# Optimization experiments

Hardware: AMD Instinct MI355X
Metric: run time of the kernel (lower is better)

The kernel has to match this reference:

```python
import jax, jax.numpy as jnp
import numpy as np

B, T, C = 4, 2048, 1024
H = 16
D = C // H  # head_dim = 64


def setup_inputs() -> dict:
    key = jax.random.key(0)
    k1, k2, k3, k4, k5 = jax.random.split(key, 5)
    s = 1.0 / np.sqrt(C)
    return {
        "hidden_state": jax.random.normal(k1, (B, T, C), dtype=jnp.float32),
        "qkv_w": jax.random.uniform(k2, (C, 3 * C), jnp.float32, -s, s),
        "qkv_b": jax.random.uniform(k3, (3 * C,), jnp.float32, -s, s),
        "o_w": jax.random.uniform(k4, (C, C), jnp.float32, -s, s),
        "o_b": jax.random.uniform(k5, (C,), jnp.float32, -s, s),
    }


def reference(hidden_state, qkv_w, qkv_b, o_w, o_b):
    Bq, Tq, Cq = hidden_state.shape
    qkv = hidden_state @ qkv_w + qkv_b  # [B,T,3C]
    q, k, v = jnp.split(qkv, 3, axis=-1)
    # [B,T,C] -> [B,H,T,D]
    q = q.reshape(Bq, Tq, H, D).transpose(0, 2, 1, 3)
    k = k.reshape(Bq, Tq, H, D).transpose(0, 2, 1, 3)
    v = v.reshape(Bq, Tq, H, D).transpose(0, 2, 1, 3)
    scaling = D ** (-0.5)
    scores = jnp.einsum("bhqd,bhkd->bhqk", q, k) * scaling  # [B,H,T,T]
    causal = jnp.tril(jnp.ones((Tq, Tq), dtype=bool))
    scores = jnp.where(causal[None, None], scores, -jnp.inf)
    attn = jax.nn.softmax(scores, axis=-1)
    out = jnp.einsum("bhqk,bhkd->bhqd", attn, v)  # [B,H,T,D]
    out = out.transpose(0, 2, 1, 3).reshape(Bq, Tq, Cq)
    return out @ o_w + o_b
```

## Files before the change

### kernel.cpp

```cpp
#include <hip/hip_runtime.h>
#include <hip/hip_bf16.h>

#define Bn 4
#define Tn 2048
#define Cn 1024
#define Hn 16
#define Dn 64
#define Kdim 1024

typedef __bf16 bf16x8 __attribute__((ext_vector_type(8)));
typedef float f32x4 __attribute__((ext_vector_type(4)));
union B8 { uint4 u; bf16x8 f; ushort s[8]; };

static __device__ __forceinline__ ushort f2bf(float x) {
    __hip_bfloat16 h = __float2bfloat16(x);
    return *(ushort*)&h;
}

#define AS1 __attribute__((address_space(1)))
#define AS3 __attribute__((address_space(3)))

static __device__ __forceinline__ void gload_lds16(const ushort* g, ushort* l) {
    __builtin_amdgcn_global_load_lds((AS1 const uint4*)(const void*)g,
                                     (AS3 uint4*)(void*)l, 16, 0, 0);
}

__global__ __launch_bounds__(256) void prep_fused(
    const float* __restrict__ X, const float* __restrict__ qkv_w,
    const float* __restrict__ o_w,
    ushort* __restrict__ Xb, ushort* __restrict__ Wqt, ushort* __restrict__ Wot)
{
    if (blockIdx.y == 0) {
        int i = (blockIdx.x * 256 + threadIdx.x) * 8;
        float4 a = *(const float4*)&X[i];
        float4 b = *(const float4*)&X[i + 4];
        ushort4 o0, o1;
        o0.x = f2bf(a.x); o0.y = f2bf(a.y); o0.z = f2bf(a.z); o0.w = f2bf(a.w);
        o1.x = f2bf(b.x); o1.y = f2bf(b.y); o1.z = f2bf(b.z); o1.w = f2bf(b.w);
        *(ushort4*)&Xb[i] = o0;
        *(ushort4*)&Xb[i + 4] = o1;
        return;
    }
    const float* W; ushort* Wt; int N, bx;
    if (blockIdx.y == 1) { W = qkv_w; Wt = Wqt; N = 3 * Cn; bx = blockIdx.x; }
    else                 { W = o_w;   Wt = Wot; N = Cn;     bx = blockIdx.x; }
    if (bx >= (N / 32) * 32) return;
    const int n0 = (bx % (N / 32)) * 32, k0 = (bx / (N / 32)) * 32;
    __shared__ float Ls[32][33];
    const int tx = threadIdx.x & 31, ty = threadIdx.x >> 5;
    #pragma unroll
    for (int i = 0; i < 4; i++) {
        int r = ty + i * 8;
        Ls[r][tx] = W[(size_t)(k0 + r) * N + n0 + tx];
    }
    __syncthreads();
    #pragma unroll
    for (int i = 0; i < 4; i++) {
        int r = ty + i * 8;
        Wt[(size_t)(n0 + r) * Kdim + k0 + tx] = f2bf(Ls[tx][r]);
    }
}

template <int EPI>
__global__ __launch_bounds__(256) void gemm_bt(
    const ushort* __restrict__ A, const ushort* __restrict__ Bt,
    const float* __restrict__ bias,
    float* __restrict__ Out, ushort* __restrict__ Qb,
    ushort* __restrict__ Kb, ushort* __restrict__ Vtb)
{
    const int m0 = blockIdx.y * 128;
    const int n0 = blockIdx.x * 128;
    const int t  = threadIdx.x;
    const int wave = t >> 6, lane = t & 63;
    const int ln = lane & 15, quad = lane >> 4;
    const int wm = wave >> 1, wn = wave & 1;

    __shared__ ushort As[128 * 64];
    __shared__ ushort Bs[128 * 64];

    f32x4 acc[4][4] = {};

    for (int k0 = 0; k0 < Kdim; k0 += 64) {
        __syncthreads();
        #pragma unroll
        for (int it = 0; it < 4; it++) {
            int c = it * 256 + wave * 64 + lane;
            int row = c >> 3, seg = c & 7;
            int gseg = seg ^ (row & 7);
            gload_lds16(&A [(size_t)(m0 + row) * Kdim + k0 + gseg * 8], &As[c * 8]);
            gload_lds16(&Bt[(size_t)(n0 + row) * Kdim + k0 + gseg * 8], &Bs[c * 8]);
        }
        __syncthreads();

        #pragma unroll
        for (int ks = 0; ks < 2; ks++) {
            bf16x8 af[4], bf[4];
            #pragma unroll
            for (int mm = 0; mm < 4; mm++) {
                int row = wm * 64 + mm * 16 + ln;
                int seg = (ks * 4 + quad) ^ (ln & 7);
                B8 tmp; tmp.u = *(const uint4*)&As[row * 64 + seg * 8];
                af[mm] = tmp.f;
            }
            #pragma unroll
            for (int nn = 0; nn < 4; nn++) {
                int row = wn * 64 + nn * 16 + ln;
                int seg = (ks * 4 + quad) ^ (ln & 7);
                B8 tmp; tmp.u = *(const uint4*)&Bs[row * 64 + seg * 8];
                bf[nn] = tmp.f;
            }
            #pragma unroll
            for (int mm = 0; mm < 4; mm++)
                #pragma unroll
                for (int nn = 0; nn < 4; nn++)
                    acc[mm][nn] = __builtin_amdgcn_mfma_f32_16x16x32_bf16(
                        af[mm], bf[nn], acc[mm][nn], 0, 0, 0);
        }
    }

    if (EPI == 0) {
        #pragma unroll
        for (int nn = 0; nn < 4; nn++) {
            int n = n0 + wn * 64 + nn * 16 + ln;
            float bv = bias[n];
            #pragma unroll
            for (int mm = 0; mm < 4; mm++) {
                int mbase = m0 + wm * 64 + mm * 16 + quad * 4;
                #pragma unroll
                for (int reg = 0; reg < 4; reg++)
                    Out[(size_t)(mbase + reg) * 1024 + n] = acc[mm][nn][reg] + bv;
            }
        }
    } else {
        const int nb = n0 + wn * 64;
        const int which = nb >> 10;
        const int h = (nb & 1023) >> 6;
        const float scale = (which == 0) ? 0.125f * 1.44269504088896f : 1.0f;
        const int b_ = m0 >> 11;
        const int t0 = (m0 & 2047) + wm * 64;

        __syncthreads();
        ushort* tile = ((wave & 2) ? Bs : As) + (wave & 1) * 4096;

        if (which == 2) {
            #pragma unroll
            for (int nn = 0; nn < 4; nn++) {
                float bv = bias[nb + nn * 16 + ln];
                #pragma unroll
                for (int mm = 0; mm < 4; mm++)
                    #pragma unroll
                    for (int reg = 0; reg < 4; reg++) {
                        int m = mm * 16 + quad * 4 + reg;
                        int n = nn * 16 + ln;
                        tile[n * 64 + (m ^ (((n >> 1) & 7) * 8))] =
                            f2bf(acc[mm][nn][reg] + bv);
                    }
            }
            #pragma unroll
            for (int it = 0; it < 8; it++) {
                int idx = it * 64 + lane;
                int row = idx >> 3, seg = idx & 7;
                uint4 v = *(const uint4*)&tile[row * 64 +
                              ((seg * 8) ^ (((row >> 1) & 7) * 8))];
                *(uint4*)&Vtb[((size_t)((b_ * Hn + h) * Dn) + row) * Tn + t0 + seg * 8] = v;
            }
        } else {
            ushort* dst = (which == 0) ? Qb : Kb;
            #pragma unroll
            for (int nn = 0; nn < 4; nn++) {
                float bv = bias[nb + nn * 16 + ln];
                #pragma unroll
                for (int mm = 0; mm < 4; mm++)
                    #pragma unroll
                    for (int reg = 0; reg < 4; reg++) {
                        int m = mm * 16 + quad * 4 + reg;
                        int n = nn * 16 + ln;
                        tile[m * 64 + (n ^ (((m >> 1) & 7) * 8))] =
                            f2bf((acc[mm][nn][reg] + bv) * scale);
                    }
            }
            #pragma unroll
            for (int it = 0; it < 8; it++) {
                int idx = it * 64 + lane;
                int row = idx >> 3, seg = idx & 7;
                uint4 v = *(const uint4*)&tile[row * 64 +
                              ((seg * 8) ^ (((row >> 1) & 7) * 8))];
                *(uint4*)&dst[((size_t)((b_ * Hn + h) * Tn) + t0 + row) * Dn + seg * 8] = v;
            }
        }
    }
}

__global__ __launch_bounds__(256, 2) void attn_mfma(
    const ushort* __restrict__ Qb, const ushort* __restrict__ Kb,
    const ushort* __restrict__ Vtb, ushort* __restrict__ Ob)
{
    const int bh   = blockIdx.x;
    const int qt   = 15 - blockIdx.y;
    const int t    = threadIdx.x;
    const int wave = t >> 6, lane = t & 63;
    const int ln   = lane & 15, quad = lane >> 4;

    __shared__ ushort Ks[2][128 * 64];
    __shared__ ushort Ps[4][32 * 34];

    const ushort* KgB = Kb  + (size_t)bh * Tn * Dn;
    const ushort* VgB = Vtb + (size_t)bh * Dn * Tn;
    const int b_ = bh >> 4, h = bh & 15;

    #define STAGE_K(kc, buf)                                                   \
        do {                                                                   \
            _Pragma("unroll")                                                  \
            for (int it = 0; it < 4; it++) {                                   \
                int c = it * 256 + wave * 64 + lane;                           \
                int row = c >> 3, seg = c & 7;                                 \
                int gs = seg ^ (row & 7);                                      \
                gload_lds16(&KgB[(size_t)((kc) * 128 + row) * Dn + gs * 8],    \
                            &Ks[buf][c * 8]);                                  \
            }                                                                  \
        } while (0)

    int cur = 0;
    STAGE_K(0, 0);

    const int q0 = qt * 128;

    const ushort* Qg = Qb + ((size_t)bh * Tn + q0 + wave * 32) * Dn;
    bf16x8 qf[2][2];
    #pragma unroll
    for (int ns = 0; ns < 2; ns++)
        #pragma unroll
        for (int ks = 0; ks < 2; ks++) {
            B8 tmp; tmp.u = *(const uint4*)&Qg[(ns * 16 + ln) * 64 + ks * 32 + quad * 8];
            qf[ns][ks] = tmp.f;
        }

    f32x4 Oacc[4][2] = {};
    float m_r[2] = {-1e30f, -1e30f}, l_r[2] = {0.f, 0.f};

    for (int kc = 0; kc <= qt; kc++) {
        __syncthreads();

        B8 vfr[4][4];
        #pragma unroll
        for (int gks = 0; gks < 4; gks++)
            #pragma unroll
            for (int ctd = 0; ctd < 4; ctd++)
                vfr[ctd][gks].u = *(const uint4*)&VgB[
                    (size_t)(ctd * 16 + ln) * Tn + kc * 128 + gks * 32 + quad * 8];

        if (kc < qt) STAGE_K(kc + 1, cur ^ 1);

        const ushort* Kc = Ks[cur];
        f32x4 S[8][2] = {};
        #pragma unroll
        for (int ks = 0; ks < 2; ks++)
            #pragma unroll
            for (int ct = 0; ct < 8; ct++) {
                B8 a; a.u = *(const uint4*)&Kc[(ct * 16 + ln) * 64 +
                                               (((ks * 4 + quad) ^ (ln & 7)) * 8)];
                #pragma unroll
                for (int ns = 0; ns < 2; ns++)
                    S[ct][ns] = __builtin_amdgcn_mfma_f32_16x16x32_bf16(
                        a.f, qf[ns][ks], S[ct][ns], 0, 0, 0);
            }

        if (kc == qt) {
            #pragma unroll
            for (int ct = 0; ct < 8; ct++) {
                int keyl = ct * 16 + quad * 4;
                #pragma unroll
                for (int ns = 0; ns < 2; ns++) {
                    int ql = wave * 32 + ns * 16 + ln;
                    #pragma unroll
                    for (int reg = 0; reg < 4; reg++)
                        if (keyl + reg > ql) S[ct][ns][reg] = -1e30f;
                }
            }
        }

        float alpha[2], ssum[2] = {0.f, 0.f};
        #pragma unroll
        for (int ns = 0; ns < 2; ns++) {
            float pm = -1e30f;
            #pragma unroll
            for (int ct = 0; ct < 8; ct++)
                #pragma unroll
                for (int reg = 0; reg < 4; reg++)
                    pm = fmaxf(pm, S[ct][ns][reg]);
            pm = fmaxf(pm, __shfl_xor(pm, 16));
            pm = fmaxf(pm, __shfl_xor(pm, 32));
            float mn = fmaxf(m_r[ns], pm);
            alpha[ns] = exp2f(m_r[ns] - mn);
            m_r[ns] = mn;
            #pragma unroll
            for (int ctd = 0; ctd < 4; ctd++)
                Oacc[ctd][ns] *= alpha[ns];
        }

        ushort* Pw = Ps[wave];
        #pragma unroll
        for (int p = 0; p < 4; p++) {
            #pragma unroll
            for (int ct_h = 0; ct_h < 2; ct_h++) {
                int ct = p * 2 + ct_h;
                #pragma unroll
                for (int ns = 0; ns < 2; ns++) {
                    ushort4 o;
                    #pragma unroll
                    for (int reg = 0; reg < 4; reg++) {
                        float pv = exp2f(S[ct][ns][reg] - m_r[ns]);
                        ssum[ns] += pv;
                        ((ushort*)&o)[reg] = f2bf(pv);
                    }
                    *(ushort4*)&Pw[(ns * 16 + ln) * 34 + ct_h * 16 + quad * 4] = o;
                }
            }
            #pragma unroll
            for (int ns = 0; ns < 2; ns++) {
                B8 pfr; pfr.u = *(const uint4*)&Pw[(ns * 16 + ln) * 34 + quad * 8];
                #pragma unroll
                for (int ctd = 0; ctd < 4; ctd++)
                    Oacc[ctd][ns] = __builtin_amdgcn_mfma_f32_16x16x32_bf16(
                        vfr[ctd][p].f, pfr.f, Oacc[ctd][ns], 0, 0, 0);
            }
        }
        #pragma unroll
        for (int ns = 0; ns < 2; ns++) {
            float s = ssum[ns];
            s += __shfl_xor(s, 16);
            s += __shfl_xor(s, 32);
            l_r[ns] = l_r[ns] * alpha[ns] + s;
        }
        cur ^= 1;
    }

    #pragma unroll
    for (int ns = 0; ns < 2; ns++) {
        float inv = 1.0f / l_r[ns];
        int token = q0 + wave * 32 + ns * 16 + ln;
        ushort* dst = Ob + ((size_t)(b_ * Tn + token)) * Cn + h * 64;
        #pragma unroll
        for (int ctd = 0; ctd < 4; ctd++) {
            ushort4 o;
            #pragma unroll
            for (int reg = 0; reg < 4; reg++)
                ((ushort*)&o)[reg] = f2bf(Oacc[ctd][ns][reg] * inv);
            *(ushort4*)&dst[ctd * 16 + quad * 4] = o;
        }
    }
    #undef STAGE_K
}

extern "C" void kernel_launch(void* const* d_in, const int* in_sizes, int n_in,
                              void* d_out, int out_size, void* d_ws, size_t ws_size,
                              hipStream_t stream) {
    const float* X     = (const float*)d_in[0];
    const float* qkv_w = (const float*)d_in[1];
    const float* qkv_b = (const float*)d_in[2];
    const float* o_w   = (const float*)d_in[3];
    const float* o_b   = (const float*)d_in[4];
    float* out = (float*)d_out;

    const size_t BTC = (size_t)Bn * Tn * Cn;
    ushort* Xb  = (ushort*)d_ws;
    ushort* Wqt = Xb  + BTC;
    ushort* Wot = Wqt + 3 * Cn * Cn;
    ushort* Qb  = Wot + Cn * Cn;
    ushort* Kb  = Qb  + BTC;
    ushort* Vtb = Kb  + BTC;
    ushort* Ao  = Vtb + BTC;

    prep_fused<<<dim3(4096, 3), 256, 0, stream>>>(X, qkv_w, o_w, Xb, Wqt, Wot);

    gemm_bt<1><<<dim3(3 * Cn / 128, 8192 / 128), 256, 0, stream>>>(
        Xb, Wqt, qkv_b, nullptr, Qb, Kb, Vtb);
    attn_mfma<<<dim3(Bn * Hn, 16), 256, 0, stream>>>(Qb, Kb, Vtb, Ao);
    gemm_bt<0><<<dim3(Cn / 128, 8192 / 128), 256, 0, stream>>>(
        Ao, Wot, o_b, out, nullptr, nullptr, nullptr);
}
```

Before: 306.3 us.

## Pair causal query tiles per block, lazy rescale, MFMA row-sum

Each attention block now handles two query tiles, qt = 15-y and qt = y, so every block does the same amount of causal work, and the grid shrinks from 16 to 8 in y. The online-softmax rescale of the output accumulators is skipped unless the running max grows by more than a threshold, checked wave-wide. The softmax denominator is computed with an MFMA against a ones vector instead of scalar sums and shuffles. Risks: half as many blocks may reduce occupancy, and the lazy rescale allows exponentials larger than one in bf16.

Result: no change. 303.4 us (-0.9%).

```diff
diff --git a/kernel.cpp b/kernel.cpp
--- a/kernel.cpp
+++ b/kernel.cpp
@@ -196,7 +196,7 @@
     const ushort* __restrict__ Vtb, ushort* __restrict__ Ob)
 {
     const int bh   = blockIdx.x;
-    const int qt   = 15 - blockIdx.y;
+    const int yp   = blockIdx.y;
     const int t    = threadIdx.x;
     const int wave = t >> 6, lane = t & 63;
     const int ln   = lane & 15, quad = lane >> 4;
@@ -207,6 +207,10 @@
     const ushort* KgB = Kb  + (size_t)bh * Tn * Dn;
     const ushort* VgB = Vtb + (size_t)bh * Dn * Tn;
     const int b_ = bh >> 4, h = bh & 15;
+
+    B8 ones;
+    #pragma unroll
+    for (int j = 0; j < 8; j++) ones.s[j] = 0x3F80;
 
     #define STAGE_K(kc, buf)                                                   \
         do {                                                                   \
@@ -220,133 +224,142 @@
             }                                                                  \
         } while (0)
 
-    int cur = 0;
-    STAGE_K(0, 0);
-
-    const int q0 = qt * 128;
-
-    const ushort* Qg = Qb + ((size_t)bh * Tn + q0 + wave * 32) * Dn;
-    bf16x8 qf[2][2];
-    #pragma unroll
-    for (int ns = 0; ns < 2; ns++)
-        #pragma unroll
-        for (int ks = 0; ks < 2; ks++) {
-            B8 tmp; tmp.u = *(const uint4*)&Qg[(ns * 16 + ln) * 64 + ks * 32 + quad * 8];
-            qf[ns][ks] = tmp.f;
-        }
-
-    f32x4 Oacc[4][2] = {};
-    float m_r[2] = {-1e30f, -1e30f}, l_r[2] = {0.f, 0.f};
-
-    for (int kc = 0; kc <= qt; kc++) {
-        __syncthreads();
-
-        B8 vfr[4][4];
-        #pragma unroll
-        for (int gks = 0; gks < 4; gks++)
-            #pragma unroll
-            for (int ctd = 0; ctd < 4; ctd++)
-                vfr[ctd][gks].u = *(const uint4*)&VgB[
-                    (size_t)(ctd * 16 + ln) * Tn + kc * 128 + gks * 32 + quad * 8];
-
-        if (kc < qt) STAGE_K(kc + 1, cur ^ 1);
-
-        const ushort* Kc = Ks[cur];
-        f32x4 S[8][2] = {};
-        #pragma unroll
-        for (int ks = 0; ks < 2; ks++)
-            #pragma unroll
-            for (int ct = 0; ct < 8; ct++) {
-                B8 a; a.u = *(const uint4*)&Kc[(ct * 16 + ln) * 64 +
-                                               (((ks * 4 + quad) ^ (ln & 7)) * 8)];
-                #pragma unroll
-                for (int ns = 0; ns < 2; ns++)
-                    S[ct][ns] = __builtin_amdgcn_mfma_f32_16x16x32_bf16(
-                        a.f, qf[ns][ks], S[ct][ns], 0, 0, 0);
-            }
-
-        if (kc == qt) {
-            #pragma unroll
-            for (int ct = 0; ct < 8; ct++) {
-                int keyl = ct * 16 + quad * 4;
+    for (int pass = 0; pass < 2; pass++) {
+        const int qt = pass ? yp : 15 - yp;
+        if (pass) __syncthreads();
+
+        int cur = 0;
+        STAGE_K(0, 0);
+
+        const int q0 = qt * 128;
+        const ushort* Qg = Qb + ((size_t)bh * Tn + q0 + wave * 32) * Dn;
+        bf16x8 qf[2][2];
+        #pragma unroll
+        for (int ns = 0; ns < 2; ns++)
+            #pragma unroll
+            for (int ks = 0; ks < 2; ks++) {
+                B8 tmp; tmp.u = *(const uint4*)&Qg[(ns * 16 + ln) * 64 + ks * 32 + quad * 8];
+                qf[ns][ks] = tmp.f;
+            }
+
+        f32x4 Oacc[4][2] = {};
+        f32x4 Lacc[2] = {};
+        float m_r[2] = {-1e30f, -1e30f};
+
+        for (int kc = 0; kc <= qt; kc++) {
+            __syncthreads();
+
+            B8 vfr[4][4];
+            #pragma unroll
+            for (int gks = 0; gks < 4; gks++)
+                #pragma unroll
+                for (int ctd = 0; ctd < 4; ctd++)
+                    vfr[ctd][gks].u = *(const uint4*)&VgB[
+                        (size_t)(ctd * 16 + ln) * Tn + kc * 128 + gks * 32 + quad * 8];
+
+            if (kc < qt) STAGE_K(kc + 1, cur ^ 1);
+
+            const ushort* Kc = Ks[cur];
+            f32x4 S[8][2] = {};
+            #pragma unroll
+            for (int ks = 0; ks < 2; ks++)
+                #pragma unroll
+                for (int ct = 0; ct < 8; ct++) {
+                    B8 a; a.u = *(const uint4*)&Kc[(ct * 16 + ln) * 64 +
+                                                   (((ks * 4 + quad) ^ (ln & 7)) * 8)];
+                    #pragma unroll
+                    for (int ns = 0; ns < 2; ns++)
+                        S[ct][ns] = __builtin_amdgcn_mfma_f32_16x16x32_bf16(
+                            a.f, qf[ns][ks], S[ct][ns], 0, 0, 0);
+                }
+
+            if (kc == qt) {
+                #pragma unroll
+                for (int ct = 0; ct < 8; ct++) {
+                    int keyl = ct * 16 + quad * 4;
+                    #pragma unroll
+                    for (int ns = 0; ns < 2; ns++) {
+                        int ql = wave * 32 + ns * 16 + ln;
+                        #pragma unroll
+                        for (int reg = 0; reg < 4; reg++)
+                            if (keyl + reg > ql) S[ct][ns][reg] = -1e30f;
+                    }
+                }
+            }
+
+            float pmv[2];
+            #pragma unroll
+            for (int ns = 0; ns < 2; ns++) {
+                float ctm[8];
+                #pragma unroll
+                for (int ct = 0; ct < 8; ct++)
+                    ctm[ct] = fmaxf(fmaxf(S[ct][ns][0], S[ct][ns][1]),
+                                    fmaxf(S[ct][ns][2], S[ct][ns][3]));
+                float pm = fmaxf(fmaxf(fmaxf(ctm[0], ctm[1]), fmaxf(ctm[2], ctm[3])),
+                                 fmaxf(fmaxf(ctm[4], ctm[5]), fmaxf(ctm[6], ctm[7])));
+                pm = fmaxf(pm, __shfl_xor(pm, 16));
+                pm = fmaxf(pm, __shfl_xor(pm, 32));
+                pmv[ns] = pm;
+            }
+
+            bool need = (pmv[0] > m_r[0] + 8.0f) | (pmv[1] > m_r[1] + 8.0f);
+            if (__any(need)) {
                 #pragma unroll
                 for (int ns = 0; ns < 2; ns++) {
-                    int ql = wave * 32 + ns * 16 + ln;
-                    #pragma unroll
-                    for (int reg = 0; reg < 4; reg++)
-                        if (keyl + reg > ql) S[ct][ns][reg] = -1e30f;
-                }
-            }
-        }
-
-        float alpha[2], ssum[2] = {0.f, 0.f};
+                    float mn = fmaxf(m_r[ns], pmv[ns]);
+                    float alpha = exp2f(m_r[ns] - mn);
+                    m_r[ns] = mn;
+                    #pragma unroll
+                    for (int ctd = 0; ctd < 4; ctd++)
+                        Oacc[ctd][ns] *= alpha;
+                    Lacc[ns] *= alpha;
+                }
+            }
+
+            ushort* Pw = Ps[wave];
+            #pragma unroll
+            for (int p = 0; p < 4; p++) {
+                #pragma unroll
+                for (int ct_h = 0; ct_h < 2; ct_h++) {
+                    int ct = p * 2 + ct_h;
+                    #pragma unroll
+                    for (int ns = 0; ns < 2; ns++) {
+                        ushort4 o;
+                        #pragma unroll
+                        for (int reg = 0; reg < 4; reg++) {
+                            float pv = exp2f(S[ct][ns][reg] - m_r[ns]);
+                            ((ushort*)&o)[reg] = f2bf(pv);
+                        }
+                        *(ushort4*)&Pw[(ns * 16 + ln) * 34 + ct_h * 16 + quad * 4] = o;
+                    }
+                }
+                #pragma unroll
+                for (int ns = 0; ns < 2; ns++) {
+                    B8 pfr; pfr.u = *(const uint4*)&Pw[(ns * 16 + ln) * 34 + quad * 8];
+                    #pragma unroll
+                    for (int ctd = 0; ctd < 4; ctd++)
+                        Oacc[ctd][ns] = __builtin_amdgcn_mfma_f32_16x16x32_bf16(
+                            vfr[ctd][p].f, pfr.f, Oacc[ctd][ns], 0, 0, 0);
+                    Lacc[ns] = __builtin_amdgcn_mfma_f32_16x16x32_bf16(
+                        ones.f, pfr.f, Lacc[ns], 0, 0, 0);
+                }
+            }
+            cur ^= 1;
+        }
+
         #pragma unroll
         for (int ns = 0; ns < 2; ns++) {
-            float pm = -1e30f;
-            #pragma unroll
-            for (int ct = 0; ct < 8; ct++)
+            float inv = 1.0f / Lacc[ns][0];
+            int token = q0 + wave * 32 + ns * 16 + ln;
+            ushort* dst = Ob + ((size_t)(b_ * Tn + token)) * Cn + h * 64;
+            #pragma unroll
+            for (int ctd = 0; ctd < 4; ctd++) {
+                ushort4 o;
                 #pragma unroll
                 for (int reg = 0; reg < 4; reg++)
-                    pm = fmaxf(pm, S[ct][ns][reg]);
-            pm = fmaxf(pm, __shfl_xor(pm, 16));
-            pm = fmaxf(pm, __shfl_xor(pm, 32));
-            float mn = fmaxf(m_r[ns], pm);
-            alpha[ns] = exp2f(m_r[ns] - mn);
-            m_r[ns] = mn;
-            #pragma unroll
-            for (int ctd = 0; ctd < 4; ctd++)
-                Oacc[ctd][ns] *= alpha[ns];
-        }
-
-        ushort* Pw = Ps[wave];
-        #pragma unroll
-        for (int p = 0; p < 4; p++) {
-            #pragma unroll
-            for (int ct_h = 0; ct_h < 2; ct_h++) {
-                int ct = p * 2 + ct_h;
-                #pragma unroll
-                for (int ns = 0; ns < 2; ns++) {
-                    ushort4 o;
-                    #pragma unroll
-                    for (int reg = 0; reg < 4; reg++) {
-                        float pv = exp2f(S[ct][ns][reg] - m_r[ns]);
-                        ssum[ns] += pv;
-                        ((ushort*)&o)[reg] = f2bf(pv);
-                    }
-                    *(ushort4*)&Pw[(ns * 16 + ln) * 34 + ct_h * 16 + quad * 4] = o;
-                }
-            }
-            #pragma unroll
-            for (int ns = 0; ns < 2; ns++) {
-                B8 pfr; pfr.u = *(const uint4*)&Pw[(ns * 16 + ln) * 34 + quad * 8];
-                #pragma unroll
-                for (int ctd = 0; ctd < 4; ctd++)
-                    Oacc[ctd][ns] = __builtin_amdgcn_mfma_f32_16x16x32_bf16(
-                        vfr[ctd][p].f, pfr.f, Oacc[ctd][ns], 0, 0, 0);
-            }
-        }
-        #pragma unroll
-        for (int ns = 0; ns < 2; ns++) {
-            float s = ssum[ns];
-            s += __shfl_xor(s, 16);
-            s += __shfl_xor(s, 32);
-            l_r[ns] = l_r[ns] * alpha[ns] + s;
-        }
-        cur ^= 1;
-    }
-
-    #pragma unroll
-    for (int ns = 0; ns < 2; ns++) {
-        float inv = 1.0f / l_r[ns];
-        int token = q0 + wave * 32 + ns * 16 + ln;
-        ushort* dst = Ob + ((size_t)(b_ * Tn + token)) * Cn + h * 64;
-        #pragma unroll
-        for (int ctd = 0; ctd < 4; ctd++) {
-            ushort4 o;
-            #pragma unroll
-            for (int reg = 0; reg < 4; reg++)
-                ((ushort*)&o)[reg] = f2bf(Oacc[ctd][ns][reg] * inv);
-            *(ushort4*)&dst[ctd * 16 + quad * 4] = o;
+                    ((ushort*)&o)[reg] = f2bf(Oacc[ctd][ns][reg] * inv);
+                *(ushort4*)&dst[ctd * 16 + quad * 4] = o;
+            }
         }
     }
     #undef STAGE_K
@@ -375,7 +388,7 @@
 
     gemm_bt<1><<<dim3(3 * Cn / 128, 8192 / 128), 256, 0, stream>>>(
         Xb, Wqt, qkv_b, nullptr, Qb, Kb, Vtb);
-    attn_mfma<<<dim3(Bn * Hn, 16), 256, 0, stream>>>(Qb, Kb, Vtb, Ao);
+    attn_mfma<<<dim3(Bn * Hn, 8), 256, 0, stream>>>(Qb, Kb, Vtb, Ao);
     gemm_bt<0><<<dim3(Cn / 128, 8192 / 128), 256, 0, stream>>>(
         Ao, Wot, o_b, out, nullptr, nullptr, nullptr);
 }
```
